# Kernel optimization log

Hardware: AMD Instinct MI355X
Metric: run time of the kernel (lower is better)

The kernel has to match this reference:

```python
import jax, jax.numpy as jnp
import numpy as np

EPS = 1e-5


def _lstm(x, W_ih, W_hh, b_ih, b_hh):
    # x: [B, T, in]; torch LSTM gate order i, f, g, o. Returns (last h, last c).
    def step(carry, xt):
        h, c = carry
        z = xt @ W_ih.T + h @ W_hh.T + (b_ih + b_hh)  # [B, 4H]
        i, f, g, o = jnp.split(z, 4, axis=-1)
        c = jax.nn.sigmoid(f) * c + jax.nn.sigmoid(i) * jnp.tanh(g)
        h = jax.nn.sigmoid(o) * jnp.tanh(c)
        return (h, c), None
    h0 = jnp.zeros((x.shape[0], W_hh.shape[1]), x.dtype)
    (h, c), _ = jax.lax.scan(step, (h0, h0), jnp.swapaxes(x, 0, 1))
    return h, c


def _bn_train(x, g, b):
    # BatchNorm1d in training mode: batch stats, biased variance.
    m = x.mean(axis=0)
    v = x.var(axis=0)
    return g * (x - m) * jax.lax.rsqrt(v + EPS) + b


def _forward(agent_traj, neighbours, aW_ih, aW_hh, ab_ih, ab_hh,
             nW_ih, nW_hh, nb_ih, nb_hh, dW_ih, dW_hh, db_ih, db_hh,
             pW, pb, rW, rb, m1W, m1b, g1, be1, m2W, m2b, g2, be2,
             i1W, i1b, ig1, ib1, i2W, i2b, ig2, ib2, segment_ids):
    B = agent_traj.shape[0]
    # relative distance: neighbour last position - owning agent's last position
    rel = neighbours[:, -1, :] - agent_traj[segment_ids, -1, :]          # [N, 2]
    agent_h, agent_c = _lstm(agent_traj, aW_ih, aW_hh, ab_ih, ab_hh)     # [B, 64]
    neigh_h, _ = _lstm(neighbours, nW_ih, nW_hh, nb_ih, nb_hh)           # [N, 64]
    rel_emb = rel @ rW.T + rb                                            # [N, 64]
    x = jnp.concatenate([neigh_h, rel_emb], axis=1)                      # [N, 128]
    x = _bn_train(jax.nn.relu(x @ m1W.T + m1b), g1, be1)                 # [N, 512]
    x = _bn_train(jax.nn.relu(x @ m2W.T + m2b), g2, be2)                 # [N, 1024]
    # per-sample max pooling over each sample's neighbours (zeros if none)
    pooled = jax.ops.segment_max(x, segment_ids, num_segments=B)         # [B, 1024]
    counts = jax.ops.segment_sum(jnp.ones((x.shape[0],), x.dtype), segment_ids, num_segments=B)
    pooled = jnp.where(counts[:, None] > 0, pooled, jnp.zeros((), x.dtype))
    d = jnp.concatenate([pooled, agent_h], axis=1)                       # [B, 1088]
    d = _bn_train(jax.nn.relu(d @ i1W.T + i1b), ig1, ib1)                # [B, 1024]
    d = _bn_train(jax.nn.relu(d @ i2W.T + i2b), ig2, ib2)                # [B, 64]

    def dec_step(carry, _):
        h, c = carry
        z = h @ dW_ih.T + h @ dW_hh.T + (db_ih + db_hh)
        i, f, g, o = jnp.split(z, 4, axis=-1)
        c = jax.nn.sigmoid(f) * c + jax.nn.sigmoid(i) * jnp.tanh(g)
        h = jax.nn.sigmoid(o) * jnp.tanh(c)
        return (h, c), h
    _, hs = jax.lax.scan(dec_step, (d, agent_c), None, length=30)        # [30, B, 64]
    pred = jnp.einsum('tbh,oh->bto', hs, pW) + pb                        # [B, 30, 2]
    return pred


def setup_inputs() -> dict:
    B, T, N, Tn, H = 2048, 20, 32768, 20, 64
    key = jax.random.key(0)
    ki = iter(jax.random.split(key, 40))
    def rn(shape, s=0.1):
        return jax.random.normal(next(ki), shape, dtype=jnp.float32) * s
    inp = dict(
        agent_traj=rn((B, T, 2), 1.0),
        neighbours=rn((N, Tn, 2), 1.0),
        aW_ih=rn((4 * H, 2)), aW_hh=rn((4 * H, H)), ab_ih=rn((4 * H,)), ab_hh=rn((4 * H,)),
        nW_ih=rn((4 * H, 2)), nW_hh=rn((4 * H, H)), nb_ih=rn((4 * H,)), nb_hh=rn((4 * H,)),
        dW_ih=rn((4 * H, H)), dW_hh=rn((4 * H, H)), db_ih=rn((4 * H,)), db_hh=rn((4 * H,)),
        pW=rn((2, H)), pb=rn((2,)),
        rW=rn((H, 2)), rb=rn((H,)),
        m1W=rn((512, 128)), m1b=rn((512,)),
        g1=jnp.ones((512,), jnp.float32), be1=jnp.zeros((512,), jnp.float32),
        m2W=rn((1024, 512)), m2b=rn((1024,)),
        g2=jnp.ones((1024,), jnp.float32), be2=jnp.zeros((1024,), jnp.float32),
        i1W=rn((1024, 1088)), i1b=rn((1024,)),
        ig1=jnp.ones((1024,), jnp.float32), ib1=jnp.zeros((1024,), jnp.float32),
        i2W=rn((H, 1024)), i2b=rn((H,)),
        ig2=jnp.ones((H,), jnp.float32), ib2=jnp.zeros((H,), jnp.float32),
        segment_ids=jnp.sort(jax.random.randint(next(ki), (N,), 0, B)).astype(jnp.int32),
    )
    return inp


def reference(agent_traj, neighbours, aW_ih, aW_hh, ab_ih, ab_hh,
              nW_ih, nW_hh, nb_ih, nb_hh, dW_ih, dW_hh, db_ih, db_hh,
              pW, pb, rW, rb, m1W, m1b, g1, be1, m2W, m2b, g2, be2,
              i1W, i1b, ig1, ib1, i2W, i2b, ig2, ib2, segment_ids):
    return _forward(agent_traj, neighbours, aW_ih, aW_hh, ab_ih, ab_hh,
                    nW_ih, nW_hh, nb_ih, nb_hh, dW_ih, dW_hh, db_ih, db_hh,
                    pW, pb, rW, rb, m1W, m1b, g1, be1, m2W, m2b, g2, be2,
                    i1W, i1b, ig1, ib1, i2W, i2b, ig2, ib2, segment_ids)
```

## Files before the change

kernel.cpp:

```cpp
#include <hip/hip_runtime.h>

#define EPS_BN 1e-5f

typedef __attribute__((ext_vector_type(8))) short short8;
typedef __attribute__((ext_vector_type(4))) float f32x4;

__device__ __forceinline__ float fast_rcp(float x) { return __builtin_amdgcn_rcpf(x); }
__device__ __forceinline__ float sigmoid_f(float x) { return fast_rcp(1.0f + __expf(-x)); }
__device__ __forceinline__ float tanh_f(float x) { return 1.0f - 2.0f * fast_rcp(__expf(2.0f * x) + 1.0f); }

__device__ __forceinline__ unsigned short f2bf(float f) {
    unsigned u = __float_as_uint(f);
    u += 0x7FFFu + ((u >> 16) & 1u);
    return (unsigned short)(u >> 16);
}
__device__ __forceinline__ unsigned pk_bf(float a, float b) {
    return (unsigned)f2bf(a) | ((unsigned)f2bf(b) << 16);
}
__device__ __forceinline__ float bf_hi(float f) {
    return __uint_as_float((unsigned)f2bf(f) << 16);
}

__device__ __forceinline__ void gload16(const unsigned short* g, unsigned short* l) {
    __builtin_amdgcn_global_load_lds(
        (const __attribute__((address_space(1))) unsigned int*)g,
        (__attribute__((address_space(3))) unsigned int*)l,
        16, 0, 0);
}

union AFrag { short e[8]; short8 v; };
union BFrag { uint4 u; short8 v; };

__global__ __launch_bounds__(256, 2) void lstm_mfma(
    const float* __restrict__ xA,
    const float* __restrict__ aW_ih, const float* __restrict__ aW_hh,
    const float* __restrict__ ab_ih, const float* __restrict__ ab_hh,
    float* __restrict__ agent_h, float* __restrict__ agent_c,
    const float* __restrict__ xN,
    const float* __restrict__ nW_ih, const float* __restrict__ nW_hh,
    const float* __restrict__ nb_ih, const float* __restrict__ nb_hh,
    const int* __restrict__ seg, const float* __restrict__ rW,
    const float* __restrict__ rb,
    unsigned short* __restrict__ x0hi, unsigned short* __restrict__ x0lo,
    int nAgentBlk, int T)
{
    __shared__ unsigned h_ex[2][2][32 * 52];

    const bool isA = (blockIdx.x < (unsigned)nAgentBlk);
    const long blk = isA ? blockIdx.x : blockIdx.x - nAgentBlk;
    const float* __restrict__ x     = isA ? xA   : xN;
    const float* __restrict__ W_ih  = isA ? aW_ih : nW_ih;
    const float* __restrict__ W_hh  = isA ? aW_hh : nW_hh;
    const float* __restrict__ b_ih  = isA ? ab_ih : nb_ih;
    const float* __restrict__ b_hh  = isA ? ab_hh : nb_hh;

    const int tid  = threadIdx.x;
    const int w    = tid >> 6;
    const int lane = tid & 63;
    const int s    = lane & 15;
    const int q    = lane >> 4;

    short8 ahi[4][3], alo[4][3];
#pragma unroll
    for (int gt = 0; gt < 4; ++gt) {
        const int n = gt * 64 + w * 16 + s;
#pragma unroll
        for (int kc = 0; kc < 2; ++kc) {
            const float* src = &W_hh[n * 64 + kc * 32 + q * 8];
            float4 v0 = *(const float4*)src;
            float4 v1 = *(const float4*)(src + 4);
            float v[8] = {v0.x, v0.y, v0.z, v0.w, v1.x, v1.y, v1.z, v1.w};
            AFrag a, b;
#pragma unroll
            for (int j = 0; j < 8; ++j) {
                a.e[j] = (short)f2bf(v[j]);
                b.e[j] = (short)f2bf(v[j] - bf_hi(v[j]));
            }
            ahi[gt][kc] = a.v;
            alo[gt][kc] = b.v;
        }
        AFrag a2, b2;
#pragma unroll
        for (int j = 0; j < 8; ++j) { a2.e[j] = 0; b2.e[j] = 0; }
        if (q == 0) {
            const float wi0 = W_ih[n * 2 + 0];
            const float wi1 = W_ih[n * 2 + 1];
            const float bs  = b_ih[n] + b_hh[n];
            a2.e[0] = (short)f2bf(wi0); b2.e[0] = (short)f2bf(wi0 - bf_hi(wi0));
            a2.e[1] = (short)f2bf(wi1); b2.e[1] = (short)f2bf(wi1 - bf_hi(wi1));
            a2.e[2] = (short)f2bf(bs);  b2.e[2] = (short)f2bf(bs  - bf_hi(bs));
        }
        ahi[gt][2] = a2.v;
        alo[gt][2] = b2.v;
    }

    for (int i = tid; i < 2 * 2 * 32 * 52; i += 256) (&h_ex[0][0][0])[i] = 0u;
    __syncthreads();
    if (tid < 32) {
        h_ex[0][0][tid * 52 + 33] = pk_bf(1.0f, 0.0f);
        h_ex[1][0][tid * 52 + 33] = pk_bf(1.0f, 0.0f);
        float2 xv = *(const float2*)&x[(blk * 32 + tid) * (long)(T * 2)];
        h_ex[0][0][tid * 52 + 32] = pk_bf(xv.x, xv.y);
        h_ex[0][1][tid * 52 + 32] = pk_bf(xv.x - bf_hi(xv.x), xv.y - bf_hi(xv.y));
    }
    __syncthreads();

    float creg[2][4] = {{0.f, 0.f, 0.f, 0.f}, {0.f, 0.f, 0.f, 0.f}};

    for (int t = 0; t < T; ++t) {
        const int rb_ = t & 1, wb = rb_ ^ 1;
        BFrag bhi[2][3], blo[2][3];
#pragma unroll
        for (int g = 0; g < 2; ++g)
#pragma unroll
        for (int kc = 0; kc < 3; ++kc) {
            const int off = (g * 16 + s) * 52 + kc * 16 + (q >> 1) * 8 + (q & 1) * 4;
            bhi[g][kc].u = *(const uint4*)&h_ex[rb_][0][off];
            blo[g][kc].u = *(const uint4*)&h_ex[rb_][1][off];
        }

        f32x4 acc[4][2];
#pragma unroll
        for (int gt = 0; gt < 4; ++gt) { acc[gt][0] = (f32x4)0.f; acc[gt][1] = (f32x4)0.f; }

#pragma unroll
        for (int kc = 0; kc < 3; ++kc) {
#pragma unroll
            for (int g = 0; g < 2; ++g) {
                const short8 bh = bhi[g][kc].v;
                const short8 bl = blo[g][kc].v;
#pragma unroll
                for (int gt = 0; gt < 4; ++gt) {
                    f32x4 a = acc[gt][g];
                    a = __builtin_amdgcn_mfma_f32_16x16x32_bf16(ahi[gt][kc], bh, a, 0, 0, 0);
                    a = __builtin_amdgcn_mfma_f32_16x16x32_bf16(ahi[gt][kc], bl, a, 0, 0, 0);
                    a = __builtin_amdgcn_mfma_f32_16x16x32_bf16(alo[gt][kc], bh, a, 0, 0, 0);
                    acc[gt][g] = a;
                }
            }
        }

#pragma unroll
        for (int g = 0; g < 2; ++g) {
            float hval[4];
#pragma unroll
            for (int r = 0; r < 4; ++r) {
                const float ei = __expf(-acc[0][g][r]);
                const float eg = __expf(2.0f * acc[2][g][r]);
                const float it = (eg - 1.0f) * fast_rcp((1.0f + ei) * (eg + 1.0f));
                const float sf = fast_rcp(1.0f + __expf(-acc[1][g][r]));
                const float c  = fmaf(sf, creg[g][r], it);
                creg[g][r] = c;
                const float eo = __expf(-acc[3][g][r]);
                const float ec = __expf(2.0f * c);
                hval[r] = (ec - 1.0f) * fast_rcp((1.0f + eo) * (ec + 1.0f));
            }
            {
                const int w0 = (g * 16 + s) * 52 + w * 8 + q * 2;
                h_ex[wb][0][w0]     = pk_bf(hval[0], hval[1]);
                h_ex[wb][0][w0 + 1] = pk_bf(hval[2], hval[3]);
                h_ex[wb][1][w0]     = pk_bf(hval[0] - bf_hi(hval[0]), hval[1] - bf_hi(hval[1]));
                h_ex[wb][1][w0 + 1] = pk_bf(hval[2] - bf_hi(hval[2]), hval[3] - bf_hi(hval[3]));
            }
            if (t == T - 1) {
                const long seq = blk * 32 + g * 16 + s;
                const int j0 = w * 16 + q * 4;
                if (isA) {
                    *(float4*)&agent_h[seq * 64 + j0] =
                        make_float4(hval[0], hval[1], hval[2], hval[3]);
                    *(float4*)&agent_c[seq * 64 + j0] =
                        make_float4(creg[g][0], creg[g][1], creg[g][2], creg[g][3]);
                } else {
                    *(uint2*)&x0hi[seq * 128 + j0] = make_uint2(
                        pk_bf(hval[0], hval[1]), pk_bf(hval[2], hval[3]));
                    *(uint2*)&x0lo[seq * 128 + j0] = make_uint2(
                        pk_bf(hval[0] - bf_hi(hval[0]), hval[1] - bf_hi(hval[1])),
                        pk_bf(hval[2] - bf_hi(hval[2]), hval[3] - bf_hi(hval[3])));
                }
            }
        }
        if (tid < 32 && t + 1 < T) {
            float2 xv = *(const float2*)&x[(blk * 32 + tid) * (long)(T * 2) + (t + 1) * 2];
            h_ex[wb][0][tid * 52 + 32] = pk_bf(xv.x, xv.y);
            h_ex[wb][1][tid * 52 + 32] = pk_bf(xv.x - bf_hi(xv.x), xv.y - bf_hi(xv.y));
        }
        __syncthreads();
    }

    if (!isA) {
        const int sloc = tid >> 3;
        const long n = blk * 32 + sloc;
        const float2 np = *(const float2*)&x[n * (long)(T * 2) + (T - 1) * 2];
        const int sid = seg[n];
        const float2 ap = *(const float2*)&xA[(long)sid * (T * 2) + (T - 1) * 2];
        const float ra = np.x - ap.x, rbv = np.y - ap.y;
        const int o0 = (tid & 7) * 8;
#pragma unroll
        for (int j = 0; j < 8; ++j) {
            const int o = o0 + j;
            const float v = fmaf(rW[o * 2 + 0], ra, fmaf(rW[o * 2 + 1], rbv, rb[o]));
            x0hi[n * 128 + 64 + o] = f2bf(v);
            x0lo[n * 128 + 64 + o] = f2bf(v - bf_hi(v));
        }
    }
}

__device__ __forceinline__ void wfrag_body(
    const float* __restrict__ W, int K, int blk, int l,
    unsigned short* __restrict__ Whi, unsigned short* __restrict__ Wlo)
{
    const int nKc = K >> 5;
    const int ti = blk / nKc, kc = blk - ti * nKc;
    const int n = ti * 16 + (l & 15);
    const int k0 = kc * 32 + (l >> 4) * 8;
    const long ob = ((long)blk * 64 + l) * 8;
#pragma unroll
    for (int j = 0; j < 8; ++j) {
        float v = W[(long)n * K + k0 + j];
        Whi[ob + j] = f2bf(v);
        Wlo[ob + j] = f2bf(v - bf_hi(v));
    }
}

__global__ __launch_bounds__(64) void prep_all(
    const float* __restrict__ m1W, const float* __restrict__ m1b,
    const float* __restrict__ i1W, const float* __restrict__ i1b,
    const float* __restrict__ dW_ih, const float* __restrict__ dW_hh,
    const float* __restrict__ db_ih, const float* __restrict__ db_hh,
    unsigned short* __restrict__ W1hi, unsigned short* __restrict__ W1lo,
    float* __restrict__ b1f,
    unsigned short* __restrict__ Wi1hi, unsigned short* __restrict__ Wi1lo,
    float* __restrict__ bi1f,
    float* __restrict__ Wc, float* __restrict__ bc)
{
    const int b = blockIdx.x, l = threadIdx.x;
    if (b < 128) {
        wfrag_body(m1W, 128, b, l, W1hi, W1lo);
    } else if (b < 2304) {
        wfrag_body(i1W, 1088, b - 128, l, Wi1hi, Wi1lo);
    } else if (b < 2312) {
        const int i = (b - 2304) * 64 + l;
        b1f[i] = m1b[i];
    } else if (b < 2328) {
        const int i = (b - 2312) * 64 + l;
        bi1f[i] = i1b[i];
    } else {
        const int idx = (b - 2328) * 64 + l;
        if (idx < 16384) Wc[idx] = dW_ih[idx] + dW_hh[idx];
        else if (idx < 16640) bc[idx - 16384] = db_ih[idx - 16384] + db_hh[idx - 16384];
    }
}

__global__ __launch_bounds__(64) void prep_w2(
    const float* __restrict__ W,
    const float* __restrict__ b2,
    const float* __restrict__ acc1,
    const float* __restrict__ g1, const float* __restrict__ be1,
    float invN,
    unsigned short* __restrict__ Whi, unsigned short* __restrict__ Wlo,
    float* __restrict__ bout)
{
    const int K = 512, nKc = 16;
    const int blk = blockIdx.x, l = threadIdx.x;
    if (blk < 1024) {
        const int ti = blk / nKc, kc = blk - ti * nKc;
        const int n = ti * 16 + (l & 15);
        const int k0 = kc * 32 + (l >> 4) * 8;
        const long ob = ((long)blk * 64 + l) * 8;
#pragma unroll
        for (int j = 0; j < 8; ++j) {
            const int k = k0 + j;
            const float mean = acc1[k] * invN;
            const float var  = acc1[512 + k] * invN - mean * mean;
            const float sc   = g1[k] * rsqrtf(var + EPS_BN);
            const float v = W[(long)n * K + k] * sc;
            Whi[ob + j] = f2bf(v);
            Wlo[ob + j] = f2bf(v - bf_hi(v));
        }
    } else {
        const int n = blk - 1024;
        float s = 0.f;
        for (int k = l; k < K; k += 64) {
            const float mean = acc1[k] * invN;
            const float var  = acc1[512 + k] * invN - mean * mean;
            const float sc   = g1[k] * rsqrtf(var + EPS_BN);
            const float sh   = be1[k] - mean * sc;
            s += sh * W[(long)n * K + k];
        }
#pragma unroll
        for (int m = 32; m >= 1; m >>= 1) s += __shfl_xor(s, m, 64);
        if (l == 0) bout[n] = b2[n] + s;
    }
}

__global__ __launch_bounds__(256, 2) void gemm_split(
    const unsigned short* __restrict__ Ahi,
    const unsigned short* __restrict__ Alo,
    const unsigned short* __restrict__ Whi,
    const unsigned short* __restrict__ Wlo,
    const float* __restrict__ bias,
    float* __restrict__ Yf,
    unsigned short* __restrict__ Yhi,
    unsigned short* __restrict__ Ylo,
    float* __restrict__ accum,
    const int* __restrict__ segp,
    float* __restrict__ poolmax,
    int M, int K, int O)
{
    __shared__ unsigned short As[2][2][128 * 32];
    __shared__ int segl[128];
    const int t = threadIdx.x;
    const int lane = t & 63;
    const int w = t >> 6;
    const int wm = w & 1, wn = w >> 1;

    const int nx = gridDim.x;
    const int flat = blockIdx.y * nx + blockIdx.x;
    const int grp = flat / (8 * nx);
    const int loc = flat - grp * (8 * nx);
    const int m0 = (grp * 8 + (loc & 7)) * 128;
    const int n0 = (loc >> 3) * 128;
    const int nKc = K >> 5;

    f32x4 acc[4][4];
#pragma unroll
    for (int mt = 0; mt < 4; ++mt)
#pragma unroll
    for (int nt = 0; nt < 4; ++nt) acc[mt][nt] = (f32x4)0.f;

    const int rloc0 = w * 32 + (lane >> 2);
    const int rloc1 = rloc0 + 16;
    const int sd = lane & 3;
    const unsigned short* gsrc[2][2];
    gsrc[0][0] = Ahi + (long)(m0 + rloc0) * K + (sd ^ ((rloc0 >> 1) & 3)) * 8;
    gsrc[0][1] = Ahi + (long)(m0 + rloc1) * K + (sd ^ ((rloc1 >> 1) & 3)) * 8;
    gsrc[1][0] = Alo + (long)(m0 + rloc0) * K + (sd ^ ((rloc0 >> 1) & 3)) * 8;
    gsrc[1][1] = Alo + (long)(m0 + rloc1) * K + (sd ^ ((rloc1 >> 1) & 3)) * 8;

    auto stageA = [&](int buf, int kc) {
#pragma unroll
        for (int pp = 0; pp < 2; ++pp)
#pragma unroll
        for (int cc = 0; cc < 2; ++cc)
            gload16(gsrc[pp][cc] + kc * 32,
                    &As[buf][pp][(w * 32 + cc * 16) * 32]);
    };

    const int s2 = ((lane >> 4) ^ ((lane >> 1) & 3)) * 8;
    const int arow = wm * 64 + (lane & 15);
    const long bt0 = (long)((n0 >> 4) + wn * 4);

    auto loadB = [&](BFrag* bh, BFrag* bl, int kc) {
#pragma unroll
        for (int nt = 0; nt < 4; ++nt) {
            const long fb = ((bt0 + nt) * nKc + kc) * 512 + lane * 8;
            bh[nt].u = *(const uint4*)(Whi + fb);
            bl[nt].u = *(const uint4*)(Wlo + fb);
        }
    };
    auto compute = [&](int buf, BFrag* bh, BFrag* bl) {
        BFrag afh[4], afl[4];
#pragma unroll
        for (int mt = 0; mt < 4; ++mt) {
            afh[mt].u = *(const uint4*)&As[buf][0][(arow + mt * 16) * 32 + s2];
            afl[mt].u = *(const uint4*)&As[buf][1][(arow + mt * 16) * 32 + s2];
        }
#pragma unroll
        for (int nt = 0; nt < 4; ++nt)
#pragma unroll
        for (int mt = 0; mt < 4; ++mt) {
            f32x4 a = acc[mt][nt];
            a = __builtin_amdgcn_mfma_f32_16x16x32_bf16(afh[mt].v, bh[nt].v, a, 0, 0, 0);
            a = __builtin_amdgcn_mfma_f32_16x16x32_bf16(afh[mt].v, bl[nt].v, a, 0, 0, 0);
            a = __builtin_amdgcn_mfma_f32_16x16x32_bf16(afl[mt].v, bh[nt].v, a, 0, 0, 0);
            acc[mt][nt] = a;
        }
    };

    BFrag bh0[4], bl0[4], bh1[4], bl1[4];
    stageA(0, 0);
    loadB(bh0, bl0, 0);
    __syncthreads();
    for (int kc = 0; kc < nKc; kc += 2) {
        stageA(1, kc + 1);
        loadB(bh1, bl1, kc + 1);
        compute(0, bh0, bl0);
        __syncthreads();
        if (kc + 2 < nKc) {
            stageA(0, kc + 2);
            loadB(bh0, bl0, kc + 2);
        }
        compute(1, bh1, bl1);
        if (kc + 2 < nKc) __syncthreads();
    }

    int sid0 = 0, span = 0;
    bool useLds = false;
    float* pool = nullptr;
    if (segp) {
        __syncthreads();
        if (t < 128) segl[t] = segp[m0 + t];
        __syncthreads();
        sid0 = segl[0];
        span = segl[127] - sid0 + 1;
        pool = (float*)&As[0][0][0];
        useLds = (span <= 60);
        if (useLds) {
            for (int i = t; i < span * 132; i += 256) pool[i] = 0.f;
            __syncthreads();
        }
    }

    const int cn = lane & 15, cq = lane >> 4;
#pragma unroll
    for (int nt = 0; nt < 4; ++nt) {
        const int cl = wn * 64 + nt * 16 + cn;
        const int n = n0 + cl;
        const float bs = bias[n];
        float s = 0.f, ssq = 0.f;
#pragma unroll
        for (int mt = 0; mt < 4; ++mt) {
            const int mb = wm * 64 + mt * 16 + cq * 4;
            float vmax = 0.f; int sid = -1;
#pragma unroll
            for (int r = 0; r < 4; ++r) {
                const float v = fmaxf(acc[mt][nt][r] + bs, 0.f);
                s += v; ssq += v * v;
                if (segp) {
                    const int sr = segl[mb + r];
                    if (r == 0) { vmax = v; sid = sr; }
                    else if (sr == sid) { vmax = fmaxf(vmax, v); }
                    else {
                        if (vmax > 0.f) {
                            if (useLds)
                                atomicMax((int*)&pool[(sid - sid0) * 132 + cl], __float_as_int(vmax));
                            else
                                atomicMax((int*)&poolmax[(long)sid * O + n], __float_as_int(vmax));
                        }
                        sid = sr; vmax = v;
                    }
                } else if (Yf) {
                    Yf[(long)(m0 + mb + r) * O + n] = v;
                } else {
                    const long idx = (long)(m0 + mb + r) * O + n;
                    Yhi[idx] = f2bf(v);
                    Ylo[idx] = f2bf(v - bf_hi(v));
                }
            }
            if (segp && vmax > 0.f) {
                if (useLds)
                    atomicMax((int*)&pool[(sid - sid0) * 132 + cl], __float_as_int(vmax));
                else
                    atomicMax((int*)&poolmax[(long)sid * O + n], __float_as_int(vmax));
            }
        }
        if (accum) {
            s   += __shfl_xor(s, 16, 64);   ssq += __shfl_xor(ssq, 16, 64);
            s   += __shfl_xor(s, 32, 64);   ssq += __shfl_xor(ssq, 32, 64);
            if (cq == 0) {
                atomicAdd(&accum[n], s);
                atomicAdd(&accum[O + n], ssq);
            }
        }
    }

    if (segp && useLds) {
        __syncthreads();
        for (int e = t; e < span * 128; e += 256) {
            const int sl = e >> 7, c = e & 127;
            const float v = pool[sl * 132 + c];
            const long gi = (long)(sid0 + sl) * O + (n0 + c);
            if (sl == 0 || sl == span - 1) {
                if (v > 0.f) atomicMax((int*)&poolmax[gi], __float_as_int(v));
            } else {
                poolmax[gi] = v;
            }
        }
    }
}

__global__ __launch_bounds__(256) void bn_finalize(
    const float* __restrict__ accum, const float* __restrict__ g,
    const float* __restrict__ be, int O, float invM,
    float* __restrict__ scale, float* __restrict__ shift)
{
    const int o = blockIdx.x * 256 + threadIdx.x;
    if (o < O) {
        const float mean = accum[o] * invM;
        const float var  = accum[O + o] * invM - mean * mean;
        const float sc   = g[o] * rsqrtf(var + EPS_BN);
        scale[o] = sc;
        shift[o] = be[o] - mean * sc;
    }
}

__global__ __launch_bounds__(256) void build_d0(
    const float* __restrict__ poolraw, const float* __restrict__ agent_h,
    const int* __restrict__ seg, int N,
    const float* __restrict__ acc2, const float* __restrict__ g2,
    const float* __restrict__ be2, float invN,
    unsigned short* __restrict__ d0hi, unsigned short* __restrict__ d0lo)
{
    const int b = blockIdx.x;
    int l = 0, h = N;
    while (l < h) { const int mid = (l + h) >> 1; if (seg[mid] < b) l = mid + 1; else h = mid; }
    const bool nonempty = (l < N) && (seg[l] == b);
    for (int c = threadIdx.x; c < 1088; c += 256) {
        float v;
        if (c < 1024) {
            const float mean = acc2[c] * invN;
            const float var  = acc2[1024 + c] * invN - mean * mean;
            const float sc   = g2[c] * rsqrtf(var + EPS_BN);
            const float sh   = be2[c] - mean * sc;
            v = nonempty ? fmaf(sc, poolraw[(long)b * 1024 + c], sh) : 0.f;
        } else {
            v = agent_h[(long)b * 64 + (c - 1024)];
        }
        d0hi[(long)b * 1088 + c] = f2bf(v);
        d0lo[(long)b * 1088 + c] = f2bf(v - bf_hi(v));
    }
}

__global__ __launch_bounds__(256) void gemm_i2_part(
    const float* __restrict__ A,
    const float* __restrict__ W,
    const float* __restrict__ ascale, const float* __restrict__ ashift,
    float* __restrict__ part, int M, int K, int kchunk)
{
    __shared__ float As[16][132];
    __shared__ float Bs[16][68];
    const int t = threadIdx.x;
    const int m0 = blockIdx.x * 128;
    const int ks = blockIdx.y;
    const int kbeg = ks * kchunk;
    const int kend = kbeg + kchunk;
    const int tm = (t & 15) * 8;
    const int tn = (t >> 4) * 4;
    const int ar = t >> 1;
    const int ac = (t & 1) * 8;
    const int br = t >> 2;
    const int bc = (t & 3) * 4;

    float acc[8][4];
#pragma unroll
    for (int i = 0; i < 8; ++i)
#pragma unroll
    for (int j = 0; j < 4; ++j) acc[i][j] = 0.f;

    for (int k0 = kbeg; k0 < kend; k0 += 16) {
        float4 a0 = *(const float4*)&A[(long)(m0+ar)*K + k0 + ac];
        float4 a1 = *(const float4*)&A[(long)(m0+ar)*K + k0 + ac + 4];
        float4 s0 = *(const float4*)&ascale[k0 + ac];
        float4 s1 = *(const float4*)&ascale[k0 + ac + 4];
        float4 h0 = *(const float4*)&ashift[k0 + ac];
        float4 h1 = *(const float4*)&ashift[k0 + ac + 4];
        a0.x = fmaf(a0.x, s0.x, h0.x); a0.y = fmaf(a0.y, s0.y, h0.y);
        a0.z = fmaf(a0.z, s0.z, h0.z); a0.w = fmaf(a0.w, s0.w, h0.w);
        a1.x = fmaf(a1.x, s1.x, h1.x); a1.y = fmaf(a1.y, s1.y, h1.y);
        a1.z = fmaf(a1.z, s1.z, h1.z); a1.w = fmaf(a1.w, s1.w, h1.w);
        float4 b0 = *(const float4*)&W[(long)br*K + k0 + bc];
        __syncthreads();
        As[ac+0][ar] = a0.x; As[ac+1][ar] = a0.y; As[ac+2][ar] = a0.z; As[ac+3][ar] = a0.w;
        As[ac+4][ar] = a1.x; As[ac+5][ar] = a1.y; As[ac+6][ar] = a1.z; As[ac+7][ar] = a1.w;
        Bs[bc+0][br] = b0.x; Bs[bc+1][br] = b0.y; Bs[bc+2][br] = b0.z; Bs[bc+3][br] = b0.w;
        __syncthreads();
#pragma unroll
        for (int kk = 0; kk < 16; ++kk) {
            float av[8], bv[4];
            *(float4*)&av[0] = *(const float4*)&As[kk][tm];
            *(float4*)&av[4] = *(const float4*)&As[kk][tm + 4];
            *(float4*)&bv[0] = *(const float4*)&Bs[kk][tn];
#pragma unroll
            for (int i = 0; i < 8; ++i)
#pragma unroll
            for (int j = 0; j < 4; ++j)
                acc[i][j] = fmaf(av[i], bv[j], acc[i][j]);
        }
    }

    float* po = part + (long)ks * M * 64;
#pragma unroll
    for (int i = 0; i < 8; ++i)
        *(float4*)&po[(long)(m0 + tm + i) * 64 + tn] = *(float4*)&acc[i][0];
}

__global__ __launch_bounds__(256) void i2_finish_stats(
    const float* __restrict__ part, const float* __restrict__ bias,
    int M, int KS, float* __restrict__ t2, float* __restrict__ accum)
{
    __shared__ float l1[256], l2[256];
    const int t = threadIdx.x;
    const long base = (long)blockIdx.x * 2048;
    float s = 0.f, ss = 0.f;
#pragma unroll
    for (int k = 0; k < 8; ++k) {
        const long idx = base + k * 256 + t;
        float v = 0.f;
        for (int ks = 0; ks < KS; ++ks) v += part[(long)ks * M * 64 + idx];
        v = fmaxf(v + bias[idx & 63], 0.f);
        t2[idx] = v;
        s += v; ss += v * v;
    }
    l1[t] = s; l2[t] = ss;
    __syncthreads();
    if (t < 64) {
        s  = l1[t] + l1[t + 64] + l1[t + 128] + l1[t + 192];
        ss = l2[t] + l2[t + 64] + l2[t + 128] + l2[t + 192];
        atomicAdd(&accum[t], s);
        atomicAdd(&accum[64 + t], ss);
    }
}

__global__ __launch_bounds__(256) void decoder_kernel(
    const float* __restrict__ t2, const float* __restrict__ acc4,
    const float* __restrict__ ig2, const float* __restrict__ ib2, float invB,
    const float* __restrict__ agent_c,
    const float* __restrict__ Wc, const float* __restrict__ bc,
    const float* __restrict__ pW, const float* __restrict__ pb,
    float* __restrict__ pred )
{
    __shared__ float h_lds[2][64];
    __shared__ float zg_lds[2][64];
    __shared__ float zo_lds[2][64];
    const int t = threadIdx.x;
    const int lane = t & 63;
    const int wave = t >> 6;
    const int s = wave >> 1;
    const int role = wave & 1;
    const long seq = (long)blockIdx.x * 2 + s;

    const int r0 = role * 128 + lane;
    const int r1 = r0 + 64;
    float w0[64], w1[64];
#pragma unroll
    for (int k = 0; k < 64; k += 4) {
        float4 va = *(const float4*)&Wc[r0 * 64 + k];
        w0[k] = va.x; w0[k+1] = va.y; w0[k+2] = va.z; w0[k+3] = va.w;
        float4 vb = *(const float4*)&Wc[r1 * 64 + k];
        w1[k] = vb.x; w1[k+1] = vb.y; w1[k+2] = vb.z; w1[k+3] = vb.w;
    }
    const float bias0 = bc[r0];
    const float bias1 = bc[r1];
    const float pw0 = pW[lane], pw1 = pW[64 + lane];
    const float pb0 = pb[0], pb1 = pb[1];

    float c = agent_c[seq*64 + lane];
    if (role == 0) {
        const float mean = acc4[lane] * invB;
        const float var  = acc4[64 + lane] * invB - mean * mean;
        const float sc   = ig2[lane] * rsqrtf(var + EPS_BN);
        const float sh   = ib2[lane] - mean * sc;
        h_lds[s][lane] = fmaf(sc, t2[seq*64 + lane], sh);
    }
    __syncthreads();
    float hv = h_lds[s][lane];

    for (int step = 0; step < 30; ++step) {
        float z0 = bias0, z1 = bias1;
#pragma unroll
        for (int k = 0; k < 64; ++k) {
            float hk = __int_as_float(__builtin_amdgcn_readlane(__float_as_int(hv), k));
            z0 = fmaf(hk, w0[k], z0);
            z1 = fmaf(hk, w1[k], z1);
        }
        if (role == 1) { zg_lds[s][lane] = z0; zo_lds[s][lane] = z1; }
        __syncthreads();
        if (role == 0) {
            const float ig = sigmoid_f(z0);
            const float fg = sigmoid_f(z1);
            const float gg = tanh_f(zg_lds[s][lane]);
            const float og = sigmoid_f(zo_lds[s][lane]);
            c = fmaf(fg, c, ig * gg);
            h_lds[s][lane] = og * tanh_f(c);
        }
        __syncthreads();
        hv = h_lds[s][lane];
        if (role == 0) {
            float p0 = hv * pw0;
            float p1 = hv * pw1;
#pragma unroll
            for (int m = 32; m >= 1; m >>= 1) {
                p0 += __shfl_xor(p0, m, 64);
                p1 += __shfl_xor(p1, m, 64);
            }
            if (lane == 0) {
                pred[seq*60 + step*2 + 0] = p0 + pb0;
                pred[seq*60 + step*2 + 1] = p1 + pb1;
            }
        }
    }
}

extern "C" void kernel_launch(void* const* d_in, const int* in_sizes, int n_in,
                              void* d_out, int out_size, void* d_ws, size_t ws_size,
                              hipStream_t stream)
{
    const float* agent_traj = (const float*)d_in[0];
    const float* neighbours = (const float*)d_in[1];
    const float* aW_ih = (const float*)d_in[2];
    const float* aW_hh = (const float*)d_in[3];
    const float* ab_ih = (const float*)d_in[4];
    const float* ab_hh = (const float*)d_in[5];
    const float* nW_ih = (const float*)d_in[6];
    const float* nW_hh = (const float*)d_in[7];
    const float* nb_ih = (const float*)d_in[8];
    const float* nb_hh = (const float*)d_in[9];
    const float* dW_ih = (const float*)d_in[10];
    const float* dW_hh = (const float*)d_in[11];
    const float* db_ih = (const float*)d_in[12];
    const float* db_hh = (const float*)d_in[13];
    const float* pW = (const float*)d_in[14];
    const float* pb = (const float*)d_in[15];
    const float* rW = (const float*)d_in[16];
    const float* rb = (const float*)d_in[17];
    const float* m1W = (const float*)d_in[18];
    const float* m1b = (const float*)d_in[19];
    const float* g1  = (const float*)d_in[20];
    const float* be1 = (const float*)d_in[21];
    const float* m2W = (const float*)d_in[22];
    const float* m2b = (const float*)d_in[23];
    const float* g2  = (const float*)d_in[24];
    const float* be2 = (const float*)d_in[25];
    const float* i1W = (const float*)d_in[26];
    const float* i1b = (const float*)d_in[27];
    const float* ig1 = (const float*)d_in[28];
    const float* ib1 = (const float*)d_in[29];
    const float* i2W = (const float*)d_in[30];
    const float* i2b = (const float*)d_in[31];
    const float* ig2 = (const float*)d_in[32];
    const float* ib2 = (const float*)d_in[33];
    const int*   seg = (const int*)d_in[34];
    float* pred = (float*)d_out;

    const int B = 2048, T = 20, N = 32768;

    char* p = (char*)d_ws;
    auto alloc = [&](size_t bytes) -> char* {
        char* r = p; p += (bytes + 255) & ~(size_t)255; return r;
    };
    float* agent_h = (float*)alloc((size_t)B*64*4);
    float* agent_c = (float*)alloc((size_t)B*64*4);
    char* neigh_region = alloc((size_t)N*64*4);
    unsigned short* x0hi = (unsigned short*)alloc((size_t)N*128*2);
    unsigned short* x0lo = (unsigned short*)alloc((size_t)N*128*2);
    char* y1hi_region  = alloc((size_t)N*512*2);
    unsigned short* y1lo = (unsigned short*)alloc((size_t)N*512*2);
    float* poolraw = (float*)alloc((size_t)B*1024*4);
    float* accAll = (float*)alloc((size_t)(1024+2048+2048+128)*4);
    float* acc1 = accAll;
    float* acc2 = accAll + 1024;
    float* acc3 = accAll + 3072;
    float* acc4 = accAll + 5120;
    float* sc3 = (float*)alloc(1024*4); float* sh3 = (float*)alloc(1024*4);
    float* Wc = (float*)alloc(256*64*4);
    float* bc = (float*)alloc(256*4);
    unsigned short* W1hi = (unsigned short*)alloc((size_t)512*128*2);
    unsigned short* W1lo = (unsigned short*)alloc((size_t)512*128*2);
    unsigned short* W2hi = (unsigned short*)alloc((size_t)1024*512*2);
    unsigned short* W2lo = (unsigned short*)alloc((size_t)1024*512*2);
    unsigned short* Wi1hi = (unsigned short*)alloc((size_t)1024*1088*2);
    unsigned short* Wi1lo = (unsigned short*)alloc((size_t)1024*1088*2);
    float* b1f = (float*)alloc(512*4);
    float* b2f = (float*)alloc(1024*4);
    float* bi1f = (float*)alloc(1024*4);
    float* i2part = (float*)alloc((size_t)8*B*64*4);

    float* t1 = (float*)neigh_region;
    unsigned short* y1hi = (unsigned short*)y1hi_region;
    unsigned short* d0hi = (unsigned short*)y1hi_region;
    unsigned short* d0lo = d0hi + (size_t)B*1088;
    float* t2 = (float*)(y1hi_region + (size_t)2*B*1088*2);

    hipMemsetAsync(accAll, 0, (1024+2048+2048+128)*sizeof(float), stream);
    hipMemsetAsync(poolraw, 0, (size_t)B*1024*4, stream);

    prep_all<<<2588, 64, 0, stream>>>(m1W, m1b, i1W, i1b, dW_ih, dW_hh, db_ih, db_hh,
                                      W1hi, W1lo, b1f, Wi1hi, Wi1lo, bi1f, Wc, bc);

    lstm_mfma<<<B/32 + N/32, 256, 0, stream>>>(
        agent_traj, aW_ih, aW_hh, ab_ih, ab_hh, agent_h, agent_c,
        neighbours, nW_ih, nW_hh, nb_ih, nb_hh,
        seg, rW, rb, x0hi, x0lo, B/32, T);

    gemm_split<<<dim3(512/128, N/128), 256, 0, stream>>>(
        x0hi, x0lo, W1hi, W1lo, b1f, nullptr, y1hi, y1lo, acc1,
        nullptr, nullptr, N, 128, 512);

    prep_w2<<<2048, 64, 0, stream>>>(m2W, m2b, acc1, g1, be1, 1.0f/N,
                                     W2hi, W2lo, b2f);

    gemm_split<<<dim3(1024/128, N/128), 256, 0, stream>>>(
        y1hi, y1lo, W2hi, W2lo, b2f, nullptr, nullptr, nullptr, acc2,
        seg, poolraw, N, 512, 1024);

    build_d0<<<B, 256, 0, stream>>>(poolraw, agent_h, seg, N, acc2, g2, be2,
                                    1.0f/N, d0hi, d0lo);

    gemm_split<<<dim3(1024/128, B/128), 256, 0, stream>>>(
        d0hi, d0lo, Wi1hi, Wi1lo, bi1f, t1, nullptr, nullptr, acc3,
        nullptr, nullptr, B, 1088, 1024);
    bn_finalize<<<4, 256, 0, stream>>>(acc3, ig1, ib1, 1024, 1.0f/B, sc3, sh3);

    gemm_i2_part<<<dim3(B/128, 8), 256, 0, stream>>>(t1, i2W, sc3, sh3, i2part,
                                                     B, 1024, 128);
    i2_finish_stats<<<64, 256, 0, stream>>>(i2part, i2b, B, 8, t2, acc4);

    decoder_kernel<<<B/2, 256, 0, stream>>>(t2, acc4, ig2, ib2, 1.0f/B,
                                            agent_c, Wc, bc, pW, pb, pred);
}
```

Measured before the change: 581.4 us.

## Triple-buffer A tiles in gemm_split with explicit vmcnt waits and barriers

Changes the GEMM main loop from a two-stage LDS double buffer to a three-stage ring. A tiles are staged two iterations ahead, and B fragments alternate between two register sets. Partial s_waitcnt vmcnt(12) waits with raw s_barrier and sched_barrier fences let loads stay in flight across iterations. The larger LDS allocation also raises the span threshold for the LDS pooling path. Costs are more shared memory per block, which may limit occupancy, and fragile hand-tuned wait counts.

```diff
diff --git a/kernel.cpp b/kernel.cpp
--- a/kernel.cpp
+++ b/kernel.cpp
@@ -307,7 +307,7 @@
     float* __restrict__ poolmax,
     int M, int K, int O)
 {
-    __shared__ unsigned short As[2][2][128 * 32];
+    __shared__ unsigned short As[3][2][128 * 32];
     __shared__ int segl[128];
     const int t = threadIdx.x;
     const int lane = t & 63;
@@ -337,13 +337,17 @@
     gsrc[1][0] = Alo + (long)(m0 + rloc0) * K + (sd ^ ((rloc0 >> 1) & 3)) * 8;
     gsrc[1][1] = Alo + (long)(m0 + rloc1) * K + (sd ^ ((rloc1 >> 1) & 3)) * 8;
 
-    auto stageA = [&](int buf, int kc) {
+    unsigned short* asBase = &As[0][0][0];
+    const unsigned PLANE = 128 * 32;
+    const unsigned BUFS  = 2 * PLANE;
+
+    auto stageA = [&](unsigned bufOff, int kc) {
 #pragma unroll
         for (int pp = 0; pp < 2; ++pp)
 #pragma unroll
         for (int cc = 0; cc < 2; ++cc)
             gload16(gsrc[pp][cc] + kc * 32,
-                    &As[buf][pp][(w * 32 + cc * 16) * 32]);
+                    asBase + bufOff + pp * PLANE + (w * 32 + cc * 16) * 32);
     };
 
     const int s2 = ((lane >> 4) ^ ((lane >> 1) & 3)) * 8;
@@ -358,12 +362,12 @@
             bl[nt].u = *(const uint4*)(Wlo + fb);
         }
     };
-    auto compute = [&](int buf, BFrag* bh, BFrag* bl) {
+    auto compute = [&](unsigned bufOff, BFrag* bh, BFrag* bl) {
         BFrag afh[4], afl[4];
 #pragma unroll
         for (int mt = 0; mt < 4; ++mt) {
-            afh[mt].u = *(const uint4*)&As[buf][0][(arow + mt * 16) * 32 + s2];
-            afl[mt].u = *(const uint4*)&As[buf][1][(arow + mt * 16) * 32 + s2];
+            afh[mt].u = *(const uint4*)(asBase + bufOff + (arow + mt * 16) * 32 + s2);
+            afl[mt].u = *(const uint4*)(asBase + bufOff + PLANE + (arow + mt * 16) * 32 + s2);
         }
 #pragma unroll
         for (int nt = 0; nt < 4; ++nt)
@@ -377,21 +381,32 @@
         }
     };
 
-    BFrag bh0[4], bl0[4], bh1[4], bl1[4];
+    BFrag bhA[4], blA[4], bhB[4], blB[4];
     stageA(0, 0);
-    loadB(bh0, bl0, 0);
-    __syncthreads();
-    for (int kc = 0; kc < nKc; kc += 2) {
-        stageA(1, kc + 1);
-        loadB(bh1, bl1, kc + 1);
-        compute(0, bh0, bl0);
-        __syncthreads();
-        if (kc + 2 < nKc) {
-            stageA(0, kc + 2);
-            loadB(bh0, bl0, kc + 2);
-        }
-        compute(1, bh1, bl1);
-        if (kc + 2 < nKc) __syncthreads();
+    stageA(BUFS, 1);
+    __builtin_amdgcn_sched_barrier(0);
+    loadB(bhA, blA, 0);
+    __builtin_amdgcn_sched_barrier(0);
+    asm volatile("s_waitcnt vmcnt(12)" ::: "memory");
+    __builtin_amdgcn_s_barrier();
+    __builtin_amdgcn_sched_barrier(0);
+
+    unsigned oc = 0, on = BUFS, op = 2 * BUFS;
+#pragma unroll 2
+    for (int kc = 0; kc < nKc; ++kc) {
+        if (kc + 2 < nKc) stageA(op, kc + 2);
+        __builtin_amdgcn_sched_barrier(0);
+        if (kc + 1 < nKc) {
+            if (kc & 1) loadB(bhA, blA, kc + 1);
+            else        loadB(bhB, blB, kc + 1);
+        }
+        __builtin_amdgcn_sched_barrier(0);
+        if (kc & 1) compute(oc, bhB, blB);
+        else        compute(oc, bhA, blA);
+        asm volatile("s_waitcnt vmcnt(12)" ::: "memory");
+        __builtin_amdgcn_s_barrier();
+        __builtin_amdgcn_sched_barrier(0);
+        const unsigned tmp = oc; oc = on; on = op; op = tmp;
     }
 
     int sid0 = 0, span = 0;
@@ -404,7 +419,7 @@
         sid0 = segl[0];
         span = segl[127] - sid0 + 1;
         pool = (float*)&As[0][0][0];
-        useLds = (span <= 60);
+        useLds = (span <= 90);
         if (useLds) {
             for (int i = t; i < span * 132; i += 256) pool[i] = 0.f;
             __syncthreads();
```

Measured after the change: 660.4 us. 13.6% more time.
